# Kernel tuning notes

Hardware: AMD Instinct MI355X
Metric: run time of the kernel (lower is better)

Reference implementation:

```python
import jax, jax.numpy as jnp
import numpy as np

B, T, V, E, H, O = 64, 2048, 50000, 256, 256, 16

def setup_inputs() -> dict:
    key = jax.random.key(0)
    ks = jax.random.split(key, 10)
    s_rnn = 1.0 / np.sqrt(H)
    s_fc1 = 1.0 / np.sqrt(H)
    s_fc2 = 1.0 / np.sqrt(H // 2)
    return {
        "x": jax.random.randint(ks[0], (B, T), 0, V, dtype=jnp.int32),
        "emb": jax.random.normal(ks[1], (V, E), dtype=jnp.float32),
        "W_ih": jax.random.uniform(ks[2], (H, E), jnp.float32, -s_rnn, s_rnn),
        "W_hh": jax.random.uniform(ks[3], (H, H), jnp.float32, -s_rnn, s_rnn),
        "b_ih": jax.random.uniform(ks[4], (H,), jnp.float32, -s_rnn, s_rnn),
        "b_hh": jax.random.uniform(ks[5], (H,), jnp.float32, -s_rnn, s_rnn),
        "fc1_w": jax.random.uniform(ks[6], (H // 2, H), jnp.float32, -s_fc1, s_fc1),
        "fc1_b": jax.random.uniform(ks[7], (H // 2,), jnp.float32, -s_fc1, s_fc1),
        "fc2_w": jax.random.uniform(ks[8], (O, H // 2), jnp.float32, -s_fc2, s_fc2),
        "fc2_b": jax.random.uniform(ks[9], (O,), jnp.float32, -s_fc2, s_fc2),
    }

def reference(x, emb, W_ih, W_hh, b_ih, b_hh, fc1_w, fc1_b, fc2_w, fc2_b):
    # Embedding lookup: [B, T, E]
    e = emb[x]
    # Precompute input-to-hidden projection for all timesteps in one big GEMM
    xh = jnp.einsum("bte,he->bth", e, W_ih) + b_ih + b_hh  # [B, T, H]
    h0 = jnp.zeros((x.shape[0], W_hh.shape[0]), dtype=e.dtype)

    def step(h, xt):  # h: [B, H], xt: [B, H]
        h = jnp.tanh(xt + h @ W_hh.T)
        return h, None

    h_last, _ = jax.lax.scan(step, h0, jnp.swapaxes(xh, 0, 1))  # final hidden [B, H]
    # Dropout is identity at inference. MLP head: fc1 -> relu -> fc2
    hid = jax.nn.relu(h_last @ fc1_w.T + fc1_b)
    return hid @ fc2_w.T + fc2_b  # [B, O]
```

## Files before the change

### kernel.cpp

```cpp
#include <hip/hip_runtime.h>
#include <hip/hip_bf16.h>


#define B_  64
#define T_  2048
#define E_  256
#define H_  256
#define O_  16
#define H2_ 128
#define CH  2
#define HP  264

typedef _Float16 f16x4 __attribute__((ext_vector_type(4)));
typedef _Float16 f16x8 __attribute__((ext_vector_type(8)));
typedef float    f32x4 __attribute__((ext_vector_type(4)));

#define LDS_BARRIER() asm volatile("s_waitcnt lgkmcnt(0)\n\ts_barrier" ::: "memory")

__device__ __forceinline__ float tanh_fast(float x) {
  const float e = __expf(2.0f * x);
  return fmaf(-2.0f, __builtin_amdgcn_rcpf(e + 1.0f), 1.0f);
}

__global__ __launch_bounds__(256) void k0_cvt(
    const float* __restrict__ W_ih, const float* __restrict__ W_hh,
    _Float16* __restrict__ Wih16, _Float16* __restrict__ Whh16) {
  const int i = (blockIdx.x * 256 + threadIdx.x) * 4;
  if (i < H_ * E_) {
    float4 a = *(const float4*)&W_ih[i];
    float4 b = *(const float4*)&W_hh[i];
    f16x4 ah, bh;
    ah[0]=(_Float16)a.x; ah[1]=(_Float16)a.y; ah[2]=(_Float16)a.z; ah[3]=(_Float16)a.w;
    bh[0]=(_Float16)b.x; bh[1]=(_Float16)b.y; bh[2]=(_Float16)b.z; bh[3]=(_Float16)b.w;
    *(f16x4*)&Wih16[i] = ah;
    *(f16x4*)&Whh16[i] = bh;
  }
}

__global__ __launch_bounds__(256) void k1_xh(
    const int* __restrict__ x, const float* __restrict__ emb,
    const _Float16* __restrict__ Wih16, const float* __restrict__ b_ih,
    const float* __restrict__ b_hh, _Float16* __restrict__ xh) {
  __shared__ _Float16 A16[64][264];
  const int tid  = threadIdx.x;
  const int w    = tid >> 6;
  const int lane = tid & 63;
  const int nl   = lane & 15;
  const int koff = (lane >> 4) << 3;
  const long r0  = (long)blockIdx.x * 64;

  {
    const int c4 = lane << 2;
#pragma unroll
    for (int it = 0; it < 16; ++it) {
      const int row = (it << 2) + w;
      const long tok = x[r0 + row];
      const float4 v = *(const float4*)&emb[tok * E_ + c4];
      f16x4 hv;
      hv[0] = (_Float16)v.x; hv[1] = (_Float16)v.y;
      hv[2] = (_Float16)v.z; hv[3] = (_Float16)v.w;
      *(f16x4*)&A16[row][c4] = hv;
    }
  }

  f16x8 bfr[4][8];
#pragma unroll
  for (int nt = 0; nt < 4; ++nt) {
    const int n = (w << 6) + (nt << 4) + nl;
#pragma unroll
    for (int kt = 0; kt < 8; ++kt)
      bfr[nt][kt] = *(const f16x8*)&Wih16[n * E_ + (kt << 5) + koff];
  }
  __syncthreads();

  f32x4 acc[4][4];
#pragma unroll
  for (int mt = 0; mt < 4; ++mt)
#pragma unroll
    for (int nt = 0; nt < 4; ++nt) acc[mt][nt] = (f32x4){};

#pragma unroll
  for (int mt = 0; mt < 4; ++mt) {
#pragma unroll
    for (int kt = 0; kt < 8; ++kt) {
      const f16x8 a = *(const f16x8*)&A16[(mt << 4) + nl][(kt << 5) + koff];
#pragma unroll
      for (int nt = 0; nt < 4; ++nt)
        acc[mt][nt] = __builtin_amdgcn_mfma_f32_16x16x32_f16(a, bfr[nt][kt], acc[mt][nt], 0, 0, 0);
    }
  }
  __syncthreads();

  {
    const int rsub = (lane >> 4) << 2;
#pragma unroll
    for (int nt = 0; nt < 4; ++nt) {
      const int n = (w << 6) + (nt << 4) + nl;
      const float bias = b_ih[n] + b_hh[n];
#pragma unroll
      for (int mt = 0; mt < 4; ++mt)
#pragma unroll
        for (int j = 0; j < 4; ++j)
          A16[(mt << 4) + rsub + j][n] = (_Float16)(acc[mt][nt][j] + bias);
    }
  }
  __syncthreads();

  {
#pragma unroll
    for (int i = 0; i < 8; ++i) {
      const int row = (w << 4) + (i << 1) + (lane >> 5);
      const int col = (lane & 31) << 3;
      *(f16x8*)&xh[(r0 + row) * H_ + col] = *(const f16x8*)&A16[row][col];
    }
  }
}

__global__ __launch_bounds__(256, 1) void k2_rnn(
    const _Float16* __restrict__ xh, const _Float16* __restrict__ Whh16,
    const float* __restrict__ fc1_w, const float* __restrict__ fc1_b,
    const float* __restrict__ fc2_w, const float* __restrict__ fc2_b,
    float* __restrict__ out) {
  __shared__ _Float16 h16[2][CH][HP];
  __shared__ float    hid_s[CH][H2_ + 4];

  const int tid  = threadIdx.x;
  const int w    = tid >> 6;
  const int lane = tid & 63;
  const int nl   = lane & 15;
  const int quad = lane >> 4;
  const int cc   = nl & 1;
  const int mts  = (nl >> 1) & 3;
  const int koff = quad << 3;
  const int rowb = (w << 6) + (mts << 4) + (quad << 2);
  const int c0   = blockIdx.x * CH;

  f16x8 afr[4][8];
#pragma unroll
  for (int mt = 0; mt < 4; ++mt) {
    const int i = (w << 6) + (mt << 4) + nl;
#pragma unroll
    for (int kt = 0; kt < 8; ++kt)
      afr[mt][kt] = *(const f16x8*)&Whh16[i * H_ + (kt << 5) + koff];
  }

  if (tid < 66) *(f16x8*)&(((_Float16*)h16[0])[tid << 3]) = (f16x8){};

  const _Float16* xb = xh + (size_t)(c0 + cc) * T_ * H_ + rowb;
  f16x4 xq[4], xn[4];
#pragma unroll
  for (int s = 0; s < 4; ++s) xq[s] = *(const f16x4*)&xb[(size_t)s * H_];
#pragma unroll
  for (int s = 0; s < 4; ++s) xn[s] = *(const f16x4*)&xb[(size_t)(4 + s) * H_];
  __syncthreads();

#define STEP(RB, WB, S)                                                        \
  {                                                                            \
    f16x8 bfr[8];                                                              \
    _Pragma("unroll")                                                          \
    for (int kt = 0; kt < 8; ++kt)                                             \
      bfr[kt] = *(const f16x8*)&h16[RB][cc][(kt << 5) + koff];                 \
    const f32x4 zz = {};                                                       \
    f32x4 sm[4];                                                               \
    _Pragma("unroll")                                                          \
    for (int mt = 0; mt < 4; ++mt) {                                           \
      f32x4 a0 = __builtin_amdgcn_mfma_f32_16x16x32_f16(afr[mt][0], bfr[0], zz, 0, 0, 0); \
      a0       = __builtin_amdgcn_mfma_f32_16x16x32_f16(afr[mt][1], bfr[1], a0, 0, 0, 0); \
      a0       = __builtin_amdgcn_mfma_f32_16x16x32_f16(afr[mt][2], bfr[2], a0, 0, 0, 0); \
      a0       = __builtin_amdgcn_mfma_f32_16x16x32_f16(afr[mt][3], bfr[3], a0, 0, 0, 0); \
      f32x4 a1 = __builtin_amdgcn_mfma_f32_16x16x32_f16(afr[mt][4], bfr[4], zz, 0, 0, 0); \
      a1       = __builtin_amdgcn_mfma_f32_16x16x32_f16(afr[mt][5], bfr[5], a1, 0, 0, 0); \
      a1       = __builtin_amdgcn_mfma_f32_16x16x32_f16(afr[mt][6], bfr[6], a1, 0, 0, 0); \
      a1       = __builtin_amdgcn_mfma_f32_16x16x32_f16(afr[mt][7], bfr[7], a1, 0, 0, 0); \
      sm[mt] = a0 + a1;                                                        \
    }                                                                          \
    f32x4 ss = sm[0];                                                          \
    _Pragma("unroll")                                                          \
    for (int m = 1; m < 4; ++m) if (mts == m) ss = sm[m];                      \
    f16x4 o;                                                                   \
    _Pragma("unroll")                                                          \
    for (int j = 0; j < 4; ++j)                                                \
      o[j] = (_Float16)tanh_fast(ss[j] + (float)xq[S][j]);                     \
    if (nl < 8) *(f16x4*)&h16[WB][cc][rowb] = o;                               \
    LDS_BARRIER();                                                             \
  }

  for (int tt = 0; tt < T_; tt += 4) {
    STEP(0, 1, 0)
    STEP(1, 0, 1)
    STEP(0, 1, 2)
    STEP(1, 0, 3)
#pragma unroll
    for (int s = 0; s < 4; ++s) xq[s] = xn[s];
    const int tn = tt + 8;
#pragma unroll
    for (int s = 0; s < 4; ++s) {
      const size_t ti = (size_t)((tn + s) & (T_ - 1)) * H_;
      xn[s] = *(const f16x4*)&xb[ti];
    }
  }
#undef STEP

  __syncthreads();

  {
    const int pc = tid >> 7;
    const int o  = tid & 127;
    float s = fc1_b[o];
#pragma unroll 8
    for (int k = 0; k < H_; ++k) s += fc1_w[o * H_ + k] * (float)h16[0][pc][k];
    hid_s[pc][o] = fmaxf(s, 0.f);
  }
  __syncthreads();
  if (tid < CH * O_) {
    const int c = tid >> 4, o = tid & 15;
    float s = fc2_b[o];
#pragma unroll 8
    for (int k = 0; k < H2_; ++k) s += fc2_w[o * H2_ + k] * hid_s[c][k];
    out[(size_t)(c0 + c) * O_ + o] = s;
  }
}

extern "C" void kernel_launch(void* const* d_in, const int* in_sizes, int n_in,
                              void* d_out, int out_size, void* d_ws, size_t ws_size,
                              hipStream_t stream) {
  const int*   x     = (const int*)d_in[0];
  const float* emb   = (const float*)d_in[1];
  const float* W_ih  = (const float*)d_in[2];
  const float* W_hh  = (const float*)d_in[3];
  const float* b_ih  = (const float*)d_in[4];
  const float* b_hh  = (const float*)d_in[5];
  const float* fc1_w = (const float*)d_in[6];
  const float* fc1_b = (const float*)d_in[7];
  const float* fc2_w = (const float*)d_in[8];
  const float* fc2_b = (const float*)d_in[9];
  float* outp = (float*)d_out;

  _Float16* xh16  = (_Float16*)d_ws;
  _Float16* Wih16 = xh16 + (size_t)B_ * T_ * H_;
  _Float16* Whh16 = Wih16 + (size_t)H_ * E_;

  k0_cvt<<<dim3(H_ * E_ / 1024), dim3(256), 0, stream>>>(W_ih, W_hh, Wih16, Whh16);
  k1_xh<<<dim3(B_ * T_ / 64), dim3(256), 0, stream>>>(x, emb, Wih16, b_ih, b_hh, xh16);
  k2_rnn<<<dim3(B_ / CH), dim3(256), 0, stream>>>(xh16, Whh16, fc1_w, fc1_b, fc2_w, fc2_b, outp);
}
```

Baseline: 1.377 ms.

## Overlap recurrence barrier with MFMAs on wave-local slice of hidden state

Restructures each recurrence step so every wave first writes its own slice of the new hidden state and immediately starts the MFMAs for the two K-tiles it produced itself, before the workgroup barrier. K-tiles are rotated per wave so those slices come first, and the remaining six tiles are read after the barrier. The input projection is now fed as the MFMA accumulator initializer rather than added after the matmul, and the two independent accumulation chains are merged into one chain interleaved across the four M-tiles. The intent is to hide barrier latency on the serial critical path, at the cost of a single longer dependent MFMA chain and a changed ordering of the floating-point sums.

```diff
diff --git a/kernel.cpp b/kernel.cpp
--- a/kernel.cpp
+++ b/kernel.cpp
@@ -138,60 +138,77 @@
   f16x8 afr[4][8];
 #pragma unroll
   for (int mt = 0; mt < 4; ++mt) {
-    const int i = (w << 6) + (mt << 4) + nl;
-#pragma unroll
-    for (int kt = 0; kt < 8; ++kt)
-      afr[mt][kt] = *(const f16x8*)&Whh16[i * H_ + (kt << 5) + koff];
-  }
-
-  if (tid < 66) *(f16x8*)&(((_Float16*)h16[0])[tid << 3]) = (f16x8){};
+    const int r = (w << 6) + (mt << 4) + nl;
+#pragma unroll
+    for (int i = 0; i < 8; ++i) {
+      const int kt = ((w << 1) + i) & 7;
+      afr[mt][i] = *(const f16x8*)&Whh16[r * H_ + (kt << 5) + koff];
+    }
+  }
+
+  const int ks0 = (w << 6) + koff;
+  const int ks1 = (w << 6) + 32 + koff;
+  int koq[6];
+#pragma unroll
+  for (int i = 0; i < 6; ++i)
+    koq[i] = ((((w << 1) + 2 + i) & 7) << 5) + koff;
 
   const _Float16* xb = xh + (size_t)(c0 + cc) * T_ * H_ + rowb;
-  f16x4 xq[4], xn[4];
-#pragma unroll
-  for (int s = 0; s < 4; ++s) xq[s] = *(const f16x4*)&xb[(size_t)s * H_];
-#pragma unroll
-  for (int s = 0; s < 4; ++s) xn[s] = *(const f16x4*)&xb[(size_t)(4 + s) * H_];
-  __syncthreads();
-
-#define STEP(RB, WB, S)                                                        \
+  f32x4 xqf[4];
+  f16x4 xn[4];
+  {
+    f16x4 x0[4];
+#pragma unroll
+    for (int s = 0; s < 4; ++s) x0[s] = *(const f16x4*)&xb[(size_t)s * H_];
+#pragma unroll
+    for (int s = 0; s < 4; ++s) xn[s] = *(const f16x4*)&xb[(size_t)(4 + s) * H_];
+#pragma unroll
+    for (int s = 0; s < 4; ++s)
+#pragma unroll
+      for (int j = 0; j < 4; ++j) xqf[s][j] = (float)x0[s][j];
+  }
+
+  f16x4 o = (f16x4){};
+
+#define BODY(P, S)                                                             \
   {                                                                            \
-    f16x8 bfr[8];                                                              \
-    _Pragma("unroll")                                                          \
-    for (int kt = 0; kt < 8; ++kt)                                             \
-      bfr[kt] = *(const f16x8*)&h16[RB][cc][(kt << 5) + koff];                 \
-    const f32x4 zz = {};                                                       \
-    f32x4 sm[4];                                                               \
-    _Pragma("unroll")                                                          \
-    for (int mt = 0; mt < 4; ++mt) {                                           \
-      f32x4 a0 = __builtin_amdgcn_mfma_f32_16x16x32_f16(afr[mt][0], bfr[0], zz, 0, 0, 0); \
-      a0       = __builtin_amdgcn_mfma_f32_16x16x32_f16(afr[mt][1], bfr[1], a0, 0, 0, 0); \
-      a0       = __builtin_amdgcn_mfma_f32_16x16x32_f16(afr[mt][2], bfr[2], a0, 0, 0, 0); \
-      a0       = __builtin_amdgcn_mfma_f32_16x16x32_f16(afr[mt][3], bfr[3], a0, 0, 0, 0); \
-      f32x4 a1 = __builtin_amdgcn_mfma_f32_16x16x32_f16(afr[mt][4], bfr[4], zz, 0, 0, 0); \
-      a1       = __builtin_amdgcn_mfma_f32_16x16x32_f16(afr[mt][5], bfr[5], a1, 0, 0, 0); \
-      a1       = __builtin_amdgcn_mfma_f32_16x16x32_f16(afr[mt][6], bfr[6], a1, 0, 0, 0); \
-      a1       = __builtin_amdgcn_mfma_f32_16x16x32_f16(afr[mt][7], bfr[7], a1, 0, 0, 0); \
-      sm[mt] = a0 + a1;                                                        \
-    }                                                                          \
-    f32x4 ss = sm[0];                                                          \
-    _Pragma("unroll")                                                          \
-    for (int m = 1; m < 4; ++m) if (mts == m) ss = sm[m];                      \
-    f16x4 o;                                                                   \
-    _Pragma("unroll")                                                          \
-    for (int j = 0; j < 4; ++j)                                                \
-      o[j] = (_Float16)tanh_fast(ss[j] + (float)xq[S][j]);                     \
-    if (nl < 8) *(f16x4*)&h16[WB][cc][rowb] = o;                               \
+    if (nl < 8) *(f16x4*)&h16[P][cc][rowb] = o;                                \
+    const f16x8 bs0 = *(const f16x8*)&h16[P][cc][ks0];                         \
+    const f16x8 bs1 = *(const f16x8*)&h16[P][cc][ks1];                         \
+    f32x4 cacc[4];                                                             \
+    _Pragma("unroll")                                                          \
+    for (int mt = 0; mt < 4; ++mt)                                             \
+      cacc[mt] = __builtin_amdgcn_mfma_f32_16x16x32_f16(afr[mt][0], bs0, xqf[S], 0, 0, 0); \
+    _Pragma("unroll")                                                          \
+    for (int mt = 0; mt < 4; ++mt)                                             \
+      cacc[mt] = __builtin_amdgcn_mfma_f32_16x16x32_f16(afr[mt][1], bs1, cacc[mt], 0, 0, 0); \
+    __builtin_amdgcn_sched_barrier(0);                                         \
     LDS_BARRIER();                                                             \
+    f16x8 bo[6];                                                               \
+    _Pragma("unroll")                                                          \
+    for (int i = 0; i < 6; ++i) bo[i] = *(const f16x8*)&h16[P][cc][koq[i]];    \
+    _Pragma("unroll")                                                          \
+    for (int i = 0; i < 6; ++i)                                                \
+      _Pragma("unroll")                                                        \
+      for (int mt = 0; mt < 4; ++mt)                                           \
+        cacc[mt] = __builtin_amdgcn_mfma_f32_16x16x32_f16(afr[mt][i + 2], bo[i], cacc[mt], 0, 0, 0); \
+    f32x4 ss = cacc[0];                                                        \
+    if (mts == 1) ss = cacc[1];                                                \
+    if (mts == 2) ss = cacc[2];                                                \
+    if (mts == 3) ss = cacc[3];                                                \
+    _Pragma("unroll")                                                          \
+    for (int j = 0; j < 4; ++j) o[j] = (_Float16)tanh_fast(ss[j]);             \
   }
 
   for (int tt = 0; tt < T_; tt += 4) {
-    STEP(0, 1, 0)
-    STEP(1, 0, 1)
-    STEP(0, 1, 2)
-    STEP(1, 0, 3)
-#pragma unroll
-    for (int s = 0; s < 4; ++s) xq[s] = xn[s];
+    BODY(0, 0)
+    BODY(1, 1)
+    BODY(0, 2)
+    BODY(1, 3)
+#pragma unroll
+    for (int s = 0; s < 4; ++s)
+#pragma unroll
+      for (int j = 0; j < 4; ++j) xqf[s][j] = (float)xn[s][j];
     const int tn = tt + 8;
 #pragma unroll
     for (int s = 0; s < 4; ++s) {
@@ -199,25 +216,26 @@
       xn[s] = *(const f16x4*)&xb[ti];
     }
   }
-#undef STEP
-
+#undef BODY
+
+  if (nl < 8) *(f16x4*)&h16[0][cc][rowb] = o;
   __syncthreads();
 
   {
     const int pc = tid >> 7;
-    const int o  = tid & 127;
-    float s = fc1_b[o];
+    const int o_ = tid & 127;
+    float s = fc1_b[o_];
 #pragma unroll 8
-    for (int k = 0; k < H_; ++k) s += fc1_w[o * H_ + k] * (float)h16[0][pc][k];
-    hid_s[pc][o] = fmaxf(s, 0.f);
+    for (int k = 0; k < H_; ++k) s += fc1_w[o_ * H_ + k] * (float)h16[0][pc][k];
+    hid_s[pc][o_] = fmaxf(s, 0.f);
   }
   __syncthreads();
   if (tid < CH * O_) {
-    const int c = tid >> 4, o = tid & 15;
-    float s = fc2_b[o];
+    const int c = tid >> 4, o_ = tid & 15;
+    float s = fc2_b[o_];
 #pragma unroll 8
-    for (int k = 0; k < H2_; ++k) s += fc2_w[o * H2_ + k] * hid_s[c][k];
-    out[(size_t)(c0 + c) * O_ + o] = s;
+    for (int k = 0; k < H2_; ++k) s += fc2_w[o_ * H2_ + k] * hid_s[c][k];
+    out[(size_t)(c0 + c) * O_ + o_] = s;
   }
 }
 
```

Result: slower. 2.182 ms (+58.5%).
